# Kernel optimization log

Hardware: AMD Instinct MI355X
Metric: run time of the kernel (lower is better)

The kernel has to match this reference:

```python
import jax, jax.numpy as jnp
import numpy as np

N, F, H, O, D = 4096, 128, 4, 64, 64


def setup_inputs() -> dict:
    key = jax.random.key(0)
    k1, k2, k3, k4, k5 = jax.random.split(key, 5)
    h = jax.random.normal(k1, (1, N, F), dtype=jnp.float32)
    # dense binary adjacency (0/1)
    a = jax.random.randint(k2, (1, N, N), 0, 2).astype(jnp.float32)
    kernel = jax.random.normal(k3, (H, F, O), dtype=jnp.float32) * 0.1
    attn_kernel = jax.random.normal(k4, (H, F, D), dtype=jnp.float32) * 0.1
    attn_kernel2 = jax.random.normal(k5, (H, F, D), dtype=jnp.float32) * 0.1
    return {"h": h, "a": a, "kernel": kernel, "attn_kernel": attn_kernel, "attn_kernel2": attn_kernel2}


def reference(h, a, kernel, attn_kernel, attn_kernel2):
    x = h[0]          # [N, F]
    adj = a[0]        # [N, N] dense 0/1 adjacency
    # per-head linear projections, vectorized over heads
    feats = jnp.einsum('nf,hfo->hno', x, kernel)          # [H, N, O]
    f_self = jnp.einsum('nf,hfd->hnd', x, attn_kernel)    # [H, N, D]
    f_other = jnp.einsum('nf,hfd->hnd', x, attn_kernel2)  # [H, N, D]
    # dense attention logits, masked BEFORE the nonlinearity (as in original)
    dense = jnp.einsum('hnd,hmd->hnm', f_self, f_other)   # [H, N, N]
    masked = adj[None] * dense
    masked = jnp.where(masked >= 0, masked, 0.2 * masked)  # LeakyReLU(0.2)
    masked = masked / jnp.sqrt(jnp.asarray(D, jnp.float32))
    neg_inf = jnp.where(adj == 0, jnp.float32(-1e9), jnp.float32(0.0))  # [N, N]
    att = jax.nn.softmax(masked + neg_inf[None], axis=-1)
    att = att * (adj != 0).astype(att.dtype)[None]
    # aggregation (dropout is identity at inference, rate=0)
    node_features = jnp.einsum('hnm,hmo->hno', att, feats)  # [H, N, O]
    node_features = jax.nn.relu(node_features)
    # zero out padding rows (all-zero input features)
    row_mask = (jnp.sum((x != 0).astype(jnp.float32), axis=-1, keepdims=True) > 0).astype(jnp.float32)  # [N, 1]
    node_features = node_features * row_mask[None]
    # concat heads along last dim -> [1, N, H*O]
    out = jnp.transpose(node_features, (1, 0, 2)).reshape(N, H * O)
    return out[None]
```

## Files before the change

kernel.cpp:

```cpp
#include <hip/hip_runtime.h>
#include <hip/hip_bf16.h>

typedef unsigned short u16;
typedef unsigned int u32;
typedef unsigned long long u64;
typedef __attribute__((ext_vector_type(8))) short bf16x8;
typedef __attribute__((ext_vector_type(4))) float f32x4;
typedef __attribute__((ext_vector_type(4))) u16 u16x4;

#define N 4096
#define F 128
#define H 4
#define O 64
#define NW (N / 64)
#define NT 16
#define QSCALE 0.18033688011112043f

__device__ inline float exp2_hw(float x) {
#if __has_builtin(__builtin_amdgcn_exp2f)
  return __builtin_amdgcn_exp2f(x);
#else
  return __expf(x * 0.6931471805599453f);
#endif
}

__device__ inline u16 f2bf(float f) {
  union { __hip_bfloat16 b; u16 u; } v;
  v.b = __float2bfloat16(f);
  return v.u;
}

__global__ __launch_bounds__(256) void prep_kernel(
    const float* __restrict__ x, const float* __restrict__ adj,
    const float* __restrict__ wv, const float* __restrict__ wq,
    const float* __restrict__ wk, u16* __restrict__ Q, u16* __restrict__ K,
    u16* __restrict__ Vt, float* __restrict__ rmask, u64* __restrict__ bits) {
  const int b = blockIdx.x;
  const int t = threadIdx.x;

  if (b < 1024) {
    const int w = t >> 6, l = t & 63;
    const int row = b * 4 + w;
    const float* ar = adj + (size_t)row * N;
    u64* br = bits + (size_t)row * NW;
#pragma unroll 4
    for (int j2 = 0; j2 < 16; j2++) {
      float4 v = *(const float4*)&ar[j2 * 256 + l * 4];
      unsigned nib = (unsigned)(v.x != 0.f) | ((unsigned)(v.y != 0.f) << 1) |
                     ((unsigned)(v.z != 0.f) << 2) | ((unsigned)(v.w != 0.f) << 3);
      u64 word = (u64)nib << ((l & 15) * 4);
      word |= __shfl_xor(word, 1);
      word |= __shfl_xor(word, 2);
      word |= __shfl_xor(word, 4);
      word |= __shfl_xor(word, 8);
      if ((l & 15) == 0) br[j2 * 4 + (l >> 4)] = word;
    }
  } else if (b < 1792) {
    __shared__ __align__(16) u16 xb[64][136];
    __shared__ __align__(16) u16 wt[64][136];
    const int pb = b - 1024;
    const int brow = (pb & 63) * 64;
    const int p = pb >> 6, h = p / 3, which = p % 3;
    const float* W = (which == 0 ? wq : which == 1 ? wk : wv) + h * F * O;

#pragma unroll
    for (int i = 0; i < 8; i++) {
      int idx = t + i * 256, r = idx >> 5, c4 = idx & 31;
      float4 v = *(const float4*)&x[(brow + r) * F + c4 * 4];
      u16x4 o4 = { f2bf(v.x), f2bf(v.y), f2bf(v.z), f2bf(v.w) };
      *(u16x4*)&xb[r][c4 * 4] = o4;
    }
#pragma unroll
    for (int i = 0; i < 8; i++) {
      int idx = t + i * 256, k = idx >> 4, n4 = idx & 15;
      float4 v = *(const float4*)&W[k * O + n4 * 4];
      wt[n4 * 4 + 0][k] = f2bf(v.x);
      wt[n4 * 4 + 1][k] = f2bf(v.y);
      wt[n4 * 4 + 2][k] = f2bf(v.z);
      wt[n4 * 4 + 3][k] = f2bf(v.w);
    }
    __syncthreads();

    const int w = t >> 6, l = t & 63;
    const int lm = l & 15, lg = l >> 4;
    const f32x4 z4 = {0.f, 0.f, 0.f, 0.f};
    bf16x8 af[4];
#pragma unroll
    for (int kc = 0; kc < 4; kc++)
      af[kc] = *(const bf16x8*)&xb[w * 16 + lm][kc * 32 + lg * 8];
    f32x4 acc[4];
#pragma unroll
    for (int ct = 0; ct < 4; ct++) {
      acc[ct] = z4;
#pragma unroll
      for (int kc = 0; kc < 4; kc++) {
        bf16x8 bfr = *(const bf16x8*)&wt[ct * 16 + lm][kc * 32 + lg * 8];
        acc[ct] = __builtin_amdgcn_mfma_f32_16x16x32_bf16(af[kc], bfr, acc[ct], 0, 0, 0);
      }
    }

    const int orow = brow + w * 16 + lg * 4;
    if (which == 0) {
      u16* dst = Q + h * N * O;
#pragma unroll
      for (int ct = 0; ct < 4; ct++)
#pragma unroll
        for (int r = 0; r < 4; r++)
          dst[(orow + r) * O + ct * 16 + lm] = f2bf(acc[ct][r] * QSCALE);
    } else if (which == 1) {
      u16* dst = K + h * N * O;
#pragma unroll
      for (int ct = 0; ct < 4; ct++)
#pragma unroll
        for (int r = 0; r < 4; r++)
          dst[(orow + r) * O + ct * 16 + lm] = f2bf(acc[ct][r]);
    } else {
      u16* dst = Vt + h * O * N;
#pragma unroll
      for (int ct = 0; ct < 4; ct++) {
        u16x4 v4 = { f2bf(acc[ct][0]), f2bf(acc[ct][1]),
                     f2bf(acc[ct][2]), f2bf(acc[ct][3]) };
        *(u16x4*)&dst[(size_t)(ct * 16 + lm) * N + orow] = v4;
      }
    }
  } else {
    int n = (b - 1792) * 256 + t;
    const float4* xr = (const float4*)(x + n * F);
    float s = 0.f;
#pragma unroll
    for (int i = 0; i < F / 4; i++) {
      float4 v = xr[i];
      s += fabsf(v.x) + fabsf(v.y) + fabsf(v.z) + fabsf(v.w);
    }
    rmask[n] = (s != 0.f) ? 1.f : 0.f;
  }
}

__global__ __launch_bounds__(512, 4) void attn_kernel(
    const u64* __restrict__ bits, const u16* __restrict__ Qg,
    const u16* __restrict__ Kg, const u16* __restrict__ Vtg,
    float* __restrict__ Opart, float* __restrict__ Spart) {
  __shared__ __align__(16) char kv[2][4][8192];
  __shared__ float Ss2[8][16];

  const int tid = threadIdx.x;
  const int w = tid >> 6, l = tid & 63;
  const int lm = l & 15, lg = l >> 4;
  const int rg = w >> 1, hc = w & 1;
  const int h = blockIdx.y;
  const int z = blockIdx.z;
  const int R0 = blockIdx.x * 64;
  const int WR0 = R0 + rg * 16;
  const int CB0 = z * 2048;

  const char* Kb = (const char*)(Kg + h * N * O);
  const char* Vb = (const char*)(Vtg + h * O * N);
  const u64* bblk = bits + (size_t)WR0 * NW;

  const int srow = w * 8 + (l >> 3);
  const int ssw = (((srow & 3) | (((srow >> 3) & 1) << 2)) << 4);
  const int scol = ((l & 7) * 16) ^ ssw;

  const int krow_base = (lm & 3) + 8 * (lm >> 2);
  const int ksw = (lm & 7) << 4;
  const int vsw = (((lm & 3) | (((lm >> 3) & 1) << 2)) << 4);

  const u16* Qh = Qg + h * N * O;
  bf16x8 qa0 = *(const bf16x8*)&Qh[(WR0 + lm) * O + lg * 8];
  bf16x8 qa1 = *(const bf16x8*)&Qh[(WR0 + lm) * O + 32 + lg * 8];

  bf16x8 ones;
#pragma unroll
  for (int i = 0; i < 8; i++) ones[i] = (short)0x3F80;

  f32x4 oacc[4];
  f32x4 lacc = {0.f, 0.f, 0.f, 0.f};
#pragma unroll
  for (int i = 0; i < 4; i++) oacc[i] = (f32x4){0.f, 0.f, 0.f, 0.f};
  const f32x4 zero4 = {0.f, 0.f, 0.f, 0.f};

  auto STAGE = [&](int b, int t) {
    __builtin_amdgcn_global_load_lds(
        (const u32*)(Kb + (size_t)(CB0 + 0 * 1024 + t * 64 + srow) * 128 + scol),
        (u32*)&kv[b][0][w * 1024], 16, 0, 0);
    __builtin_amdgcn_global_load_lds(
        (const u32*)(Kb + (size_t)(CB0 + 1 * 1024 + t * 64 + srow) * 128 + scol),
        (u32*)&kv[b][1][w * 1024], 16, 0, 0);
    __builtin_amdgcn_global_load_lds(
        (const u32*)(Vb + (size_t)srow * (N * 2) + (CB0 + 0 * 1024 + t * 64) * 2 + scol),
        (u32*)&kv[b][2][w * 1024], 16, 0, 0);
    __builtin_amdgcn_global_load_lds(
        (const u32*)(Vb + (size_t)srow * (N * 2) + (CB0 + 1 * 1024 + t * 64) * 2 + scol),
        (u32*)&kv[b][3][w * 1024], 16, 0, 0);
  };

  STAGE(0, 0);
  __syncthreads();

  int b = 0;
#pragma unroll 1
  for (int t = 0; t < NT; ++t) {
    if (t + 1 < NT) STAGE(b ^ 1, t + 1);

    const int widx = (CB0 >> 6) + hc * NT + t;

    u64 word = bblk[lm * NW + widx];
    u64 w2 = word >> (8 * lg);

    const char* Kt = &kv[b][hc][0];
    f32x4 sacc[4];
    __builtin_amdgcn_s_setprio(1);
#pragma unroll
    for (int tt = 0; tt < 4; tt++) {
      const int row = krow_base + 4 * (tt & 1) + 32 * (tt >> 1);
      bf16x8 kb0 = *(const bf16x8*)(Kt + row * 128 + ((lg * 16) ^ ksw));
      bf16x8 kb1 = *(const bf16x8*)(Kt + row * 128 + ((lg * 16 + 64) ^ ksw));
      f32x4 s0 = __builtin_amdgcn_mfma_f32_16x16x32_bf16(kb0, qa0, zero4, 0, 0, 0);
      sacc[tt] = __builtin_amdgcn_mfma_f32_16x16x32_bf16(kb1, qa1, s0, 0, 0, 0);
    }
    __builtin_amdgcn_s_setprio(0);

    float pv[4][4];
#pragma unroll
    for (int tt = 0; tt < 4; tt++) {
#pragma unroll
      for (int r = 0; r < 4; r++) {
        unsigned bit = (unsigned)(w2 >> (4 * (tt & 1) + 32 * (tt >> 1) + r)) & 1u;
        float sv = sacc[tt][r];
        float lv = fmaxf(sv, 0.2f * sv);
        pv[tt][r] = bit ? exp2_hw(lv) : 0.f;
      }
    }
    bf16x8 pa0, pa1;
#pragma unroll
    for (int r = 0; r < 4; r++) {
      pa0[r]     = (short)f2bf(pv[0][r]);
      pa0[4 + r] = (short)f2bf(pv[1][r]);
      pa1[r]     = (short)f2bf(pv[2][r]);
      pa1[4 + r] = (short)f2bf(pv[3][r]);
    }

    const char* Vt_ = &kv[b][2 + hc][0];
    __builtin_amdgcn_s_setprio(1);
#pragma unroll
    for (int ot = 0; ot < 4; ot++) {
      const int o = ot * 16 + lm;
      bf16x8 vb0 = *(const bf16x8*)(Vt_ + o * 128 + ((lg * 16) ^ vsw));
      bf16x8 vb1 = *(const bf16x8*)(Vt_ + o * 128 + ((lg * 16 + 64) ^ vsw));
      oacc[ot] = __builtin_amdgcn_mfma_f32_16x16x32_bf16(vb0, pa0, oacc[ot], 0, 0, 0);
      oacc[ot] = __builtin_amdgcn_mfma_f32_16x16x32_bf16(vb1, pa1, oacc[ot], 0, 0, 0);
    }
    lacc = __builtin_amdgcn_mfma_f32_16x16x32_bf16(ones, pa0, lacc, 0, 0, 0);
    lacc = __builtin_amdgcn_mfma_f32_16x16x32_bf16(ones, pa1, lacc, 0, 0, 0);
    __builtin_amdgcn_s_setprio(0);

    __syncthreads();
    b ^= 1;
  }

  float (*Om2)[64][68] = (float (*)[64][68])&kv[0][0][0];
#pragma unroll
  for (int ot = 0; ot < 4; ot++)
    *(f32x4*)&Om2[hc][rg * 16 + lm][ot * 16 + lg * 4] = oacc[ot];
  if (lg == 0) Ss2[w][lm] = lacc[0];
  __syncthreads();

  const int row = tid >> 3;
  const int c0 = (tid & 7) * 8;
  const int grow = R0 + row;
  float* op = &Opart[(((size_t)z * H + h) * N + grow) * O + c0];
#pragma unroll
  for (int j = 0; j < 8; j++)
    op[j] = Om2[0][row][c0 + j] + Om2[1][row][c0 + j];
  if ((tid & 7) == 0) {
    const int rg2 = row >> 4, ri = row & 15;
    Spart[((size_t)z * H + h) * N + grow] = Ss2[rg2 * 2 + 0][ri] + Ss2[rg2 * 2 + 1][ri];
  }
}

__global__ __launch_bounds__(256) void merge_kernel(
    const float* __restrict__ Opart, const float* __restrict__ Spart,
    const float* __restrict__ rowmask, float* __restrict__ out) {
  const int h = blockIdx.y;
  const int idx = blockIdx.x * 256 + threadIdx.x;
  const int row = idx >> 4, c0 = (idx & 15) * 4;
  float S = Spart[(size_t)h * N + row] + Spart[((size_t)H + h) * N + row];
  float inv = (S > 0.f) ? 1.f / S : 0.f;
  float rm = rowmask[row];
  const float4 o0 = *(const float4*)&Opart[((size_t)h * N + row) * O + c0];
  const float4 o1 = *(const float4*)&Opart[(((size_t)H + h) * N + row) * O + c0];
  float4 r;
  r.x = fmaxf((o0.x + o1.x) * inv, 0.f) * rm;
  r.y = fmaxf((o0.y + o1.y) * inv, 0.f) * rm;
  r.z = fmaxf((o0.z + o1.z) * inv, 0.f) * rm;
  r.w = fmaxf((o0.w + o1.w) * inv, 0.f) * rm;
  *(float4*)&out[(size_t)row * (H * O) + h * O + c0] = r;
}

extern "C" void kernel_launch(void* const* d_in, const int* in_sizes, int n_in,
                              void* d_out, int out_size, void* d_ws, size_t ws_size,
                              hipStream_t stream) {
  const float* x   = (const float*)d_in[0];
  const float* adj = (const float*)d_in[1];
  const float* wv  = (const float*)d_in[2];
  const float* wq  = (const float*)d_in[3];
  const float* wk  = (const float*)d_in[4];
  float* out = (float*)d_out;

  u16* Q  = (u16*)d_ws;
  u16* K  = Q + H * N * O;
  u16* Vt = K + H * N * O;
  float* rmask = (float*)(Vt + H * N * O);
  u64* bits = (u64*)(rmask + N);
  float* Opart = (float*)(bits + (size_t)N * NW);
  float* Spart = Opart + (size_t)2 * H * N * O;

  prep_kernel<<<dim3(1808), 256, 0, stream>>>(x, adj, wv, wq, wk, Q, K, Vt, rmask, bits);
  attn_kernel<<<dim3(N / 64, H, 2), 512, 0, stream>>>(bits, Q, K, Vt, Opart, Spart);
  merge_kernel<<<dim3(N * O / 4 / 256, H), 256, 0, stream>>>(Opart, Spart, rmask, out);
}
```

Before: 67.44 us.

## Process two query row tiles per wave and split keys four ways

Each wave now handles 32 query rows instead of 16, so every K/V tile staged in LDS feeds twice as many MFMAs. The block covers 128 rows and the key dimension is split four ways instead of two, which keeps the grid size the same. Partial outputs are written as bf16 to halve partial-sum traffic, and the merge kernel now sums four partials. The trade-off is higher register pressure from doubled accumulators, plus some precision loss from storing partials in bf16.

New measurement: 66.85 us. Within noise of the previous version (-0.9%).

```diff
diff --git a/kernel.cpp b/kernel.cpp
--- a/kernel.cpp
+++ b/kernel.cpp
@@ -13,7 +13,8 @@
 #define H 4
 #define O 64
 #define NW (N / 64)
-#define NT 16
+#define NT 8
+#define NZ 4
 #define QSCALE 0.18033688011112043f
 
 __device__ inline float exp2_hw(float x) {
@@ -28,6 +29,10 @@
   union { __hip_bfloat16 b; u16 u; } v;
   v.b = __float2bfloat16(f);
   return v.u;
+}
+
+__device__ inline float bf2f(u16 u) {
+  union { float f; u32 i; } v; v.i = ((u32)u) << 16; return v.f;
 }
 
 __global__ __launch_bounds__(256) void prep_kernel(
@@ -139,9 +144,9 @@
 __global__ __launch_bounds__(512, 4) void attn_kernel(
     const u64* __restrict__ bits, const u16* __restrict__ Qg,
     const u16* __restrict__ Kg, const u16* __restrict__ Vtg,
-    float* __restrict__ Opart, float* __restrict__ Spart) {
+    u16* __restrict__ Opart, float* __restrict__ Spart) {
   __shared__ __align__(16) char kv[2][4][8192];
-  __shared__ float Ss2[8][16];
+  __shared__ float Ss2[8][32];
 
   const int tid = threadIdx.x;
   const int w = tid >> 6, l = tid & 63;
@@ -149,9 +154,9 @@
   const int rg = w >> 1, hc = w & 1;
   const int h = blockIdx.y;
   const int z = blockIdx.z;
-  const int R0 = blockIdx.x * 64;
-  const int WR0 = R0 + rg * 16;
-  const int CB0 = z * 2048;
+  const int R0 = blockIdx.x * 128;
+  const int WR0 = R0 + rg * 32;
+  const int CB0 = z * 1024;
 
   const char* Kb = (const char*)(Kg + h * N * O);
   const char* Vb = (const char*)(Vtg + h * O * N);
@@ -168,29 +173,34 @@
   const u16* Qh = Qg + h * N * O;
   bf16x8 qa0 = *(const bf16x8*)&Qh[(WR0 + lm) * O + lg * 8];
   bf16x8 qa1 = *(const bf16x8*)&Qh[(WR0 + lm) * O + 32 + lg * 8];
+  bf16x8 qb0 = *(const bf16x8*)&Qh[(WR0 + 16 + lm) * O + lg * 8];
+  bf16x8 qb1 = *(const bf16x8*)&Qh[(WR0 + 16 + lm) * O + 32 + lg * 8];
 
   bf16x8 ones;
 #pragma unroll
   for (int i = 0; i < 8; i++) ones[i] = (short)0x3F80;
 
-  f32x4 oacc[4];
-  f32x4 lacc = {0.f, 0.f, 0.f, 0.f};
-#pragma unroll
-  for (int i = 0; i < 4; i++) oacc[i] = (f32x4){0.f, 0.f, 0.f, 0.f};
+  f32x4 oaccA[4], oaccB[4];
+  f32x4 laccA = {0.f, 0.f, 0.f, 0.f}, laccB = {0.f, 0.f, 0.f, 0.f};
+#pragma unroll
+  for (int i = 0; i < 4; i++) {
+    oaccA[i] = (f32x4){0.f, 0.f, 0.f, 0.f};
+    oaccB[i] = (f32x4){0.f, 0.f, 0.f, 0.f};
+  }
   const f32x4 zero4 = {0.f, 0.f, 0.f, 0.f};
 
   auto STAGE = [&](int b, int t) {
     __builtin_amdgcn_global_load_lds(
-        (const u32*)(Kb + (size_t)(CB0 + 0 * 1024 + t * 64 + srow) * 128 + scol),
+        (const u32*)(Kb + (size_t)(CB0 + 0 * 512 + t * 64 + srow) * 128 + scol),
         (u32*)&kv[b][0][w * 1024], 16, 0, 0);
     __builtin_amdgcn_global_load_lds(
-        (const u32*)(Kb + (size_t)(CB0 + 1 * 1024 + t * 64 + srow) * 128 + scol),
+        (const u32*)(Kb + (size_t)(CB0 + 1 * 512 + t * 64 + srow) * 128 + scol),
         (u32*)&kv[b][1][w * 1024], 16, 0, 0);
     __builtin_amdgcn_global_load_lds(
-        (const u32*)(Vb + (size_t)srow * (N * 2) + (CB0 + 0 * 1024 + t * 64) * 2 + scol),
+        (const u32*)(Vb + (size_t)srow * (N * 2) + (CB0 + 0 * 512 + t * 64) * 2 + scol),
         (u32*)&kv[b][2][w * 1024], 16, 0, 0);
     __builtin_amdgcn_global_load_lds(
-        (const u32*)(Vb + (size_t)srow * (N * 2) + (CB0 + 1 * 1024 + t * 64) * 2 + scol),
+        (const u32*)(Vb + (size_t)srow * (N * 2) + (CB0 + 1 * 512 + t * 64) * 2 + scol),
         (u32*)&kv[b][3][w * 1024], 16, 0, 0);
   };
 
@@ -202,42 +212,66 @@
   for (int t = 0; t < NT; ++t) {
     if (t + 1 < NT) STAGE(b ^ 1, t + 1);
 
-    const int widx = (CB0 >> 6) + hc * NT + t;
-
-    u64 word = bblk[lm * NW + widx];
-    u64 w2 = word >> (8 * lg);
+    const int widx = z * 16 + hc * NT + t;
+
+    u64 wordA = bblk[lm * NW + widx];
+    u64 wordB = bblk[(16 + lm) * NW + widx];
+    u64 wA = wordA >> (8 * lg);
+    u64 wB = wordB >> (8 * lg);
 
     const char* Kt = &kv[b][hc][0];
-    f32x4 sacc[4];
+    f32x4 sA[4], sB[4];
     __builtin_amdgcn_s_setprio(1);
 #pragma unroll
     for (int tt = 0; tt < 4; tt++) {
       const int row = krow_base + 4 * (tt & 1) + 32 * (tt >> 1);
       bf16x8 kb0 = *(const bf16x8*)(Kt + row * 128 + ((lg * 16) ^ ksw));
       bf16x8 kb1 = *(const bf16x8*)(Kt + row * 128 + ((lg * 16 + 64) ^ ksw));
-      f32x4 s0 = __builtin_amdgcn_mfma_f32_16x16x32_bf16(kb0, qa0, zero4, 0, 0, 0);
-      sacc[tt] = __builtin_amdgcn_mfma_f32_16x16x32_bf16(kb1, qa1, s0, 0, 0, 0);
+      f32x4 t0 = __builtin_amdgcn_mfma_f32_16x16x32_bf16(kb0, qa0, zero4, 0, 0, 0);
+      sA[tt] = __builtin_amdgcn_mfma_f32_16x16x32_bf16(kb1, qa1, t0, 0, 0, 0);
+      f32x4 t1 = __builtin_amdgcn_mfma_f32_16x16x32_bf16(kb0, qb0, zero4, 0, 0, 0);
+      sB[tt] = __builtin_amdgcn_mfma_f32_16x16x32_bf16(kb1, qb1, t1, 0, 0, 0);
     }
     __builtin_amdgcn_s_setprio(0);
 
-    float pv[4][4];
-#pragma unroll
-    for (int tt = 0; tt < 4; tt++) {
+    bf16x8 paA0, paA1, paB0, paB1;
+    {
+      float pv[4][4];
+#pragma unroll
+      for (int tt = 0; tt < 4; tt++)
+#pragma unroll
+        for (int r = 0; r < 4; r++) {
+          unsigned bit = (unsigned)(wA >> (4 * (tt & 1) + 32 * (tt >> 1) + r)) & 1u;
+          float sv = sA[tt][r];
+          float lv = fmaxf(sv, 0.2f * sv);
+          pv[tt][r] = bit ? exp2_hw(lv) : 0.f;
+        }
 #pragma unroll
       for (int r = 0; r < 4; r++) {
-        unsigned bit = (unsigned)(w2 >> (4 * (tt & 1) + 32 * (tt >> 1) + r)) & 1u;
-        float sv = sacc[tt][r];
-        float lv = fmaxf(sv, 0.2f * sv);
-        pv[tt][r] = bit ? exp2_hw(lv) : 0.f;
+        paA0[r]     = (short)f2bf(pv[0][r]);
+        paA0[4 + r] = (short)f2bf(pv[1][r]);
+        paA1[r]     = (short)f2bf(pv[2][r]);
+        paA1[4 + r] = (short)f2bf(pv[3][r]);
       }
     }
-    bf16x8 pa0, pa1;
-#pragma unroll
-    for (int r = 0; r < 4; r++) {
-      pa0[r]     = (short)f2bf(pv[0][r]);
-      pa0[4 + r] = (short)f2bf(pv[1][r]);
-      pa1[r]     = (short)f2bf(pv[2][r]);
-      pa1[4 + r] = (short)f2bf(pv[3][r]);
+    {
+      float pv[4][4];
+#pragma unroll
+      for (int tt = 0; tt < 4; tt++)
+#pragma unroll
+        for (int r = 0; r < 4; r++) {
+          unsigned bit = (unsigned)(wB >> (4 * (tt & 1) + 32 * (tt >> 1) + r)) & 1u;
+          float sv = sB[tt][r];
+          float lv = fmaxf(sv, 0.2f * sv);
+          pv[tt][r] = bit ? exp2_hw(lv) : 0.f;
+        }
+#pragma unroll
+      for (int r = 0; r < 4; r++) {
+        paB0[r]     = (short)f2bf(pv[0][r]);
+        paB0[4 + r] = (short)f2bf(pv[1][r]);
+        paB1[r]     = (short)f2bf(pv[2][r]);
+        paB1[4 + r] = (short)f2bf(pv[3][r]);
+      }
     }
 
     const char* Vt_ = &kv[b][2 + hc][0];
@@ -247,53 +281,78 @@
       const int o = ot * 16 + lm;
       bf16x8 vb0 = *(const bf16x8*)(Vt_ + o * 128 + ((lg * 16) ^ vsw));
       bf16x8 vb1 = *(const bf16x8*)(Vt_ + o * 128 + ((lg * 16 + 64) ^ vsw));
-      oacc[ot] = __builtin_amdgcn_mfma_f32_16x16x32_bf16(vb0, pa0, oacc[ot], 0, 0, 0);
-      oacc[ot] = __builtin_amdgcn_mfma_f32_16x16x32_bf16(vb1, pa1, oacc[ot], 0, 0, 0);
-    }
-    lacc = __builtin_amdgcn_mfma_f32_16x16x32_bf16(ones, pa0, lacc, 0, 0, 0);
-    lacc = __builtin_amdgcn_mfma_f32_16x16x32_bf16(ones, pa1, lacc, 0, 0, 0);
+      oaccA[ot] = __builtin_amdgcn_mfma_f32_16x16x32_bf16(vb0, paA0, oaccA[ot], 0, 0, 0);
+      oaccA[ot] = __builtin_amdgcn_mfma_f32_16x16x32_bf16(vb1, paA1, oaccA[ot], 0, 0, 0);
+      oaccB[ot] = __builtin_amdgcn_mfma_f32_16x16x32_bf16(vb0, paB0, oaccB[ot], 0, 0, 0);
+      oaccB[ot] = __builtin_amdgcn_mfma_f32_16x16x32_bf16(vb1, paB1, oaccB[ot], 0, 0, 0);
+    }
+    laccA = __builtin_amdgcn_mfma_f32_16x16x32_bf16(ones, paA0, laccA, 0, 0, 0);
+    laccA = __builtin_amdgcn_mfma_f32_16x16x32_bf16(ones, paA1, laccA, 0, 0, 0);
+    laccB = __builtin_amdgcn_mfma_f32_16x16x32_bf16(ones, paB0, laccB, 0, 0, 0);
+    laccB = __builtin_amdgcn_mfma_f32_16x16x32_bf16(ones, paB1, laccB, 0, 0, 0);
     __builtin_amdgcn_s_setprio(0);
 
     __syncthreads();
     b ^= 1;
   }
 
-  float (*Om2)[64][68] = (float (*)[64][68])&kv[0][0][0];
-#pragma unroll
-  for (int ot = 0; ot < 4; ot++)
-    *(f32x4*)&Om2[hc][rg * 16 + lm][ot * 16 + lg * 4] = oacc[ot];
-  if (lg == 0) Ss2[w][lm] = lacc[0];
+  float (*Om2)[128][64] = (float (*)[128][64])&kv[0][0][0];
+#pragma unroll
+  for (int ot = 0; ot < 4; ot++) {
+    *(f32x4*)&Om2[hc][rg * 32 + lm][ot * 16 + lg * 4] = oaccA[ot];
+    *(f32x4*)&Om2[hc][rg * 32 + 16 + lm][ot * 16 + lg * 4] = oaccB[ot];
+  }
+  if (lg == 0) {
+    Ss2[w][lm] = laccA[0];
+    Ss2[w][16 + lm] = laccB[0];
+  }
   __syncthreads();
 
-  const int row = tid >> 3;
-  const int c0 = (tid & 7) * 8;
-  const int grow = R0 + row;
-  float* op = &Opart[(((size_t)z * H + h) * N + grow) * O + c0];
-#pragma unroll
-  for (int j = 0; j < 8; j++)
-    op[j] = Om2[0][row][c0 + j] + Om2[1][row][c0 + j];
-  if ((tid & 7) == 0) {
-    const int rg2 = row >> 4, ri = row & 15;
-    Spart[((size_t)z * H + h) * N + grow] = Ss2[rg2 * 2 + 0][ri] + Ss2[rg2 * 2 + 1][ri];
+#pragma unroll
+  for (int rr = 0; rr < 2; rr++) {
+    const int row = rr * 64 + (tid >> 3);
+    const int c0 = (tid & 7) * 8;
+    const int grow = R0 + row;
+    u16* op = &Opart[(((size_t)z * H + h) * N + grow) * O + c0];
+    u16x4 v0 = { f2bf(Om2[0][row][c0 + 0] + Om2[1][row][c0 + 0]),
+                 f2bf(Om2[0][row][c0 + 1] + Om2[1][row][c0 + 1]),
+                 f2bf(Om2[0][row][c0 + 2] + Om2[1][row][c0 + 2]),
+                 f2bf(Om2[0][row][c0 + 3] + Om2[1][row][c0 + 3]) };
+    u16x4 v1 = { f2bf(Om2[0][row][c0 + 4] + Om2[1][row][c0 + 4]),
+                 f2bf(Om2[0][row][c0 + 5] + Om2[1][row][c0 + 5]),
+                 f2bf(Om2[0][row][c0 + 6] + Om2[1][row][c0 + 6]),
+                 f2bf(Om2[0][row][c0 + 7] + Om2[1][row][c0 + 7]) };
+    *(u16x4*)&op[0] = v0;
+    *(u16x4*)&op[4] = v1;
+    if ((tid & 7) == 0) {
+      const int rg2 = row >> 5, ri = row & 31;
+      Spart[((size_t)z * H + h) * N + grow] = Ss2[rg2 * 2 + 0][ri] + Ss2[rg2 * 2 + 1][ri];
+    }
   }
 }
 
 __global__ __launch_bounds__(256) void merge_kernel(
-    const float* __restrict__ Opart, const float* __restrict__ Spart,
+    const u16* __restrict__ Opart, const float* __restrict__ Spart,
     const float* __restrict__ rowmask, float* __restrict__ out) {
   const int h = blockIdx.y;
   const int idx = blockIdx.x * 256 + threadIdx.x;
   const int row = idx >> 4, c0 = (idx & 15) * 4;
-  float S = Spart[(size_t)h * N + row] + Spart[((size_t)H + h) * N + row];
+  float S = 0.f;
+#pragma unroll
+  for (int z = 0; z < NZ; z++) S += Spart[((size_t)z * H + h) * N + row];
   float inv = (S > 0.f) ? 1.f / S : 0.f;
   float rm = rowmask[row];
-  const float4 o0 = *(const float4*)&Opart[((size_t)h * N + row) * O + c0];
-  const float4 o1 = *(const float4*)&Opart[(((size_t)H + h) * N + row) * O + c0];
+  float a0 = 0.f, a1 = 0.f, a2 = 0.f, a3 = 0.f;
+#pragma unroll
+  for (int z = 0; z < NZ; z++) {
+    u16x4 v = *(const u16x4*)&Opart[(((size_t)z * H + h) * N + row) * O + c0];
+    a0 += bf2f(v[0]); a1 += bf2f(v[1]); a2 += bf2f(v[2]); a3 += bf2f(v[3]);
+  }
   float4 r;
-  r.x = fmaxf((o0.x + o1.x) * inv, 0.f) * rm;
-  r.y = fmaxf((o0.y + o1.y) * inv, 0.f) * rm;
-  r.z = fmaxf((o0.z + o1.z) * inv, 0.f) * rm;
-  r.w = fmaxf((o0.w + o1.w) * inv, 0.f) * rm;
+  r.x = fmaxf(a0 * inv, 0.f) * rm;
+  r.y = fmaxf(a1 * inv, 0.f) * rm;
+  r.z = fmaxf(a2 * inv, 0.f) * rm;
+  r.w = fmaxf(a3 * inv, 0.f) * rm;
   *(float4*)&out[(size_t)row * (H * O) + h * O + c0] = r;
 }
 
@@ -312,10 +371,10 @@
   u16* Vt = K + H * N * O;
   float* rmask = (float*)(Vt + H * N * O);
   u64* bits = (u64*)(rmask + N);
-  float* Opart = (float*)(bits + (size_t)N * NW);
-  float* Spart = Opart + (size_t)2 * H * N * O;
+  u16* Opart = (u16*)(bits + (size_t)N * NW);
+  float* Spart = (float*)(Opart + (size_t)NZ * H * N * O);
 
   prep_kernel<<<dim3(1808), 256, 0, stream>>>(x, adj, wv, wq, wk, Q, K, Vt, rmask, bits);
-  attn_kernel<<<dim3(N / 64, H, 2), 512, 0, stream>>>(bits, Q, K, Vt, Opart, Spart);
+  attn_kernel<<<dim3(N / 128, H, NZ), 512, 0, stream>>>(bits, Q, K, Vt, Opart, Spart);
   merge_kernel<<<dim3(N * O / 4 / 256, H), 256, 0, stream>>>(Opart, Spart, rmask, out);
 }
```
